# Optimization experiments

Hardware: AMD Instinct MI355X
Metric: run time of the kernel (lower is better)

The kernel has to match this reference:

```python
import jax, jax.numpy as jnp
import numpy as np

E = 1024
H = 8
D = E // H
WINDOW = 256
EPS = 1e-5


def layernorm(x, w, b):
    mu = jnp.mean(x, axis=-1, keepdims=True)
    var = jnp.mean((x - mu) ** 2, axis=-1, keepdims=True)
    return (x - mu) * jax.lax.rsqrt(var + EPS) * w + b


def setup_inputs() -> dict:
    key = jax.random.key(0)
    ks = jax.random.split(key, 12)
    B, T = 2, 2048
    s = 1.0 / np.sqrt(E)
    return {
        "x": jax.random.normal(ks[0], (B, T, E), jnp.float32),
        "ln1_w": jnp.ones((E,), jnp.float32),
        "ln1_b": jnp.zeros((E,), jnp.float32),
        "ln2_w": jnp.ones((E,), jnp.float32),
        "ln2_b": jnp.zeros((E,), jnp.float32),
        "in_proj_w": jax.random.normal(ks[1], (3 * E, E), jnp.float32) * s,
        "in_proj_b": jnp.zeros((3 * E,), jnp.float32),
        "out_w": jax.random.normal(ks[2], (E, E), jnp.float32) * s,
        "out_b": jnp.zeros((E,), jnp.float32),
        "w1": jax.random.normal(ks[3], (4 * E, E), jnp.float32) * s,
        "b1": jnp.zeros((4 * E,), jnp.float32),
        "w2": jax.random.normal(ks[4], (E, 4 * E), jnp.float32) * (1.0 / np.sqrt(4 * E)),
        "b2": jnp.zeros((E,), jnp.float32),
    }


def reference(x, ln1_w, ln1_b, ln2_w, ln2_b, in_proj_w, in_proj_b, out_w, out_b, w1, b1, w2, b2):
    B, T, _ = x.shape
    h = layernorm(x, ln1_w, ln1_b)
    # qkv projection: torch Linear is x @ W.T + b
    qkv = h @ in_proj_w.T + in_proj_b  # [B,T,3E]
    q, k, v = jnp.split(qkv, 3, axis=-1)
    q = q.reshape(B, T, H, D).transpose(0, 2, 1, 3)  # [B,H,T,D]
    k = k.reshape(B, T, H, D).transpose(0, 2, 1, 3)
    v = v.reshape(B, T, H, D).transpose(0, 2, 1, 3)
    scores = jnp.einsum("bhqd,bhkd->bhqk", q, k) / np.sqrt(D)
    idx = jnp.arange(T)
    row = idx[:, None]
    col = idx[None, :]
    # masked where future (col>row) OR outside window (col < row - WINDOW)
    allowed = (col <= row) & (col >= row - WINDOW)
    scores = jnp.where(allowed, scores, -jnp.inf)
    attn = jax.nn.softmax(scores, axis=-1)
    out = jnp.einsum("bhqk,bhkd->bhqd", attn, v)  # [B,H,T,D]
    out = out.transpose(0, 2, 1, 3).reshape(B, T, E)
    out = out @ out_w.T + out_b
    h2 = x + out
    m = layernorm(h2, ln2_w, ln2_b)
    m = jax.nn.relu(m @ w1.T + b1) @ w2.T + b2
    return h2 + m
```

## Files before the change

### kernel.cpp

```cpp
#include <hip/hip_runtime.h>

#define TOK 4096
#define EMB 1024

typedef __attribute__((ext_vector_type(8))) short s16x8;
typedef __attribute__((ext_vector_type(4))) float f32x4;

__device__ __forceinline__ unsigned short f2bf(float f) {
  union { float f; unsigned int u; } v; v.f = f;
  unsigned int r = v.u + 0x7FFFu + ((v.u >> 16) & 1u);
  return (unsigned short)(r >> 16);
}
__device__ __forceinline__ float bf2f(unsigned short u) {
  union { unsigned int u; float f; } v; v.u = ((unsigned int)u) << 16; return v.f;
}

#define GLOAD_LDS16(g, l) __builtin_amdgcn_global_load_lds( \
    (const __attribute__((address_space(1))) void*)(g), \
    (__attribute__((address_space(3))) void*)(l), 16, 0, 0)

template<int RELU, int PART, int NT>
__global__ __launch_bounds__(512)
void gemm256(const unsigned short* __restrict__ A,
             const unsigned short* __restrict__ B,
             const float* __restrict__ bias,
             unsigned short* __restrict__ C, int M, int N, int K)
{
  __shared__ unsigned short lds[2][2][128 * 128];
  const int tid = threadIdx.x;
  const int lane = tid & 63;
  const int w = tid >> 6;
  const int wr = w >> 2, wc = w & 3;
  const int l15 = lane & 15, lhi = lane >> 4;
  const int nbm = M >> 8;
  const int bm = blockIdx.x % nbm, bn = blockIdx.x / nbm;
  const int m0 = bm << 8, n0 = bn << 8;
  const int k0 = blockIdx.y * (NT * 64);

  const char* Abase = (const char*)(A + (size_t)m0 * K) + (size_t)k0 * 2;
  const char* Bbase = (const char*)(B + (size_t)n0 * K) + (size_t)k0 * 2;
  const size_t rowb = (size_t)K * 2;

  const int srt = tid >> 3;
  const int sccx = ((tid & 7) << 4) ^ ((srt & 7) << 4);
  const char* gA = Abase + (size_t)srt * rowb + sccx;
  const char* gB = Bbase + (size_t)srt * rowb + sccx;

  auto STAGE_A = [&](int ktl, int h, int p) {
    char* d = (char*)&lds[0][0][0] + p * 32768 + h * 16384 + (w << 10);
    const char* g = gA + (size_t)(h * 128) * rowb + ktl * 128;
    GLOAD_LDS16(g, d);
    GLOAD_LDS16(g + 64 * rowb, d + 8192);
  };
  auto STAGE_B = [&](int ktl, int h, int p) {
    char* d = (char*)&lds[1][0][0] + p * 32768 + h * 16384 + (w << 10);
    const char* g = gB + (size_t)(h * 128) * rowb + ktl * 128;
    GLOAD_LDS16(g, d);
    GLOAD_LDS16(g + 64 * rowb, d + 8192);
  };

  const int rdxor = (l15 & 7) << 4;
  const char* pA0 = (const char*)&lds[0][0][0] + (wr * 128 + l15) * 128 + ((0 * 64 + lhi * 16) ^ rdxor);
  const char* pA1 = (const char*)&lds[0][0][0] + (wr * 128 + l15) * 128 + ((1 * 64 + lhi * 16) ^ rdxor);
  const char* pB0 = (const char*)&lds[1][0][0] + (wc * 64 + l15) * 128 + ((0 * 64 + lhi * 16) ^ rdxor);
  const char* pB1 = (const char*)&lds[1][0][0] + (wc * 64 + l15) * 128 + ((1 * 64 + lhi * 16) ^ rdxor);

  f32x4 acc[8][4];
#pragma unroll
  for (int mf = 0; mf < 8; ++mf)
#pragma unroll
    for (int nf = 0; nf < 4; ++nf)
#pragma unroll
      for (int j = 0; j < 4; ++j) acc[mf][nf][j] = 0.f;

  STAGE_A(0, 0, 0); STAGE_A(0, 1, 0);
  STAGE_B(0, 0, 0); STAGE_B(0, 1, 0);
  STAGE_A(1, 0, 1); STAGE_A(1, 1, 1);
  STAGE_B(1, 0, 1);
  asm volatile("s_waitcnt vmcnt(6)" ::: "memory");
  __builtin_amdgcn_s_barrier();

  s16x8 af[8][2], bf[4][2];

#pragma unroll
  for (int kt = 0; kt < NT; ++kt) {
    const int P = (kt & 1) << 15;
    const int p = kt & 1;

#pragma unroll
    for (int mi = 0; mi < 4; ++mi) {
      af[mi][0] = *(const s16x8*)(pA0 + mi * 2048 + P);
      af[mi][1] = *(const s16x8*)(pA1 + mi * 2048 + P);
    }
#pragma unroll
    for (int ni = 0; ni < 2; ++ni) {
      bf[ni][0] = *(const s16x8*)(pB0 + ni * 2048 + P);
      bf[ni][1] = *(const s16x8*)(pB1 + ni * 2048 + P);
    }
#pragma unroll
    for (int mi = 4; mi < 8; ++mi) {
      af[mi][0] = *(const s16x8*)(pA0 + mi * 2048 + P);
      af[mi][1] = *(const s16x8*)(pA1 + mi * 2048 + P);
    }
#pragma unroll
    for (int ni = 2; ni < 4; ++ni) {
      bf[ni][0] = *(const s16x8*)(pB0 + ni * 2048 + P);
      bf[ni][1] = *(const s16x8*)(pB1 + ni * 2048 + P);
    }

    if (kt + 1 < NT) STAGE_B(kt + 1, 1, p ^ 1);

    __builtin_amdgcn_s_setprio(1);
#pragma unroll
    for (int mi = 0; mi < 4; ++mi)
#pragma unroll
      for (int ni = 0; ni < 2; ++ni)
#pragma unroll
        for (int ks = 0; ks < 2; ++ks)
          acc[mi][ni] = __builtin_amdgcn_mfma_f32_16x16x32_bf16(af[mi][ks], bf[ni][ks], acc[mi][ni], 0, 0, 0);
#pragma unroll
    for (int mi = 4; mi < 8; ++mi)
#pragma unroll
      for (int ni = 0; ni < 2; ++ni)
#pragma unroll
        for (int ks = 0; ks < 2; ++ks)
          acc[mi][ni] = __builtin_amdgcn_mfma_f32_16x16x32_bf16(af[mi][ks], bf[ni][ks], acc[mi][ni], 0, 0, 0);
#pragma unroll
    for (int mi = 0; mi < 4; ++mi)
#pragma unroll
      for (int ni = 2; ni < 4; ++ni)
#pragma unroll
        for (int ks = 0; ks < 2; ++ks)
          acc[mi][ni] = __builtin_amdgcn_mfma_f32_16x16x32_bf16(af[mi][ks], bf[ni][ks], acc[mi][ni], 0, 0, 0);
#pragma unroll
    for (int mi = 4; mi < 8; ++mi)
#pragma unroll
      for (int ni = 2; ni < 4; ++ni)
#pragma unroll
        for (int ks = 0; ks < 2; ++ks)
          acc[mi][ni] = __builtin_amdgcn_mfma_f32_16x16x32_bf16(af[mi][ks], bf[ni][ks], acc[mi][ni], 0, 0, 0);
    __builtin_amdgcn_s_setprio(0);

    __builtin_amdgcn_s_barrier();

    if (kt + 2 < NT) {
      STAGE_A(kt + 2, 0, p);
      STAGE_A(kt + 2, 1, p);
      STAGE_B(kt + 2, 0, p);
    }

    if (kt + 1 < NT) {
      if (kt + 2 < NT) asm volatile("s_waitcnt vmcnt(6)" ::: "memory");
      else             asm volatile("s_waitcnt vmcnt(0)" ::: "memory");
      __builtin_amdgcn_s_barrier();
    }
  }

  unsigned short* Cw = PART ? C + (size_t)blockIdx.y * M * N : C;
#pragma unroll
  for (int mf = 0; mf < 8; ++mf) {
    const int row = m0 + wr * 128 + mf * 16 + lhi * 4;
#pragma unroll
    for (int nf = 0; nf < 4; ++nf) {
      const int col = n0 + wc * 64 + nf * 16 + l15;
      const float bv = PART ? 0.f : bias[col];
#pragma unroll
      for (int j = 0; j < 4; ++j) {
        float v = acc[mf][nf][j] + bv;
        if (RELU) v = fmaxf(v, 0.f);
        Cw[(size_t)(row + j) * N + col] = f2bf(v);
      }
    }
  }
}

__global__ __launch_bounds__(256)
void reduce_add(const unsigned short* __restrict__ part, const float* __restrict__ res,
                const float* __restrict__ bias, float* __restrict__ out,
                int MN, int N, int S)
{
  const int i4 = (blockIdx.x * 256 + threadIdx.x) * 4;
  if (i4 >= MN) return;
  const int col = i4 & (N - 1);
  float4 v = *(const float4*)(res + i4);
  v.x += bias[col]; v.y += bias[col + 1]; v.z += bias[col + 2]; v.w += bias[col + 3];
  for (int s = 0; s < S; ++s) {
    const ushort4 p = *(const ushort4*)(part + (size_t)s * MN + i4);
    v.x += bf2f(p.x); v.y += bf2f(p.y); v.z += bf2f(p.z); v.w += bf2f(p.w);
  }
  *(float4*)(out + i4) = v;
}

__global__ __launch_bounds__(256)
void reduce_ln(const unsigned short* __restrict__ part, const float* __restrict__ x,
               const float* __restrict__ ob, const float* __restrict__ ln_w,
               const float* __restrict__ ln_b, float* __restrict__ h2,
               unsigned short* __restrict__ m_in, int S)
{
  const int row = blockIdx.x;
  const int t = threadIdx.x;
  const size_t off = (size_t)row * EMB + t * 4;
  float4 v = *(const float4*)(x + off);
  const float4 obv = ((const float4*)ob)[t];
  v.x += obv.x; v.y += obv.y; v.z += obv.z; v.w += obv.w;
  for (int s = 0; s < S; ++s) {
    const ushort4 p = *(const ushort4*)(part + (size_t)s * TOK * EMB + off);
    v.x += bf2f(p.x); v.y += bf2f(p.y); v.z += bf2f(p.z); v.w += bf2f(p.w);
  }
  *(float4*)(h2 + off) = v;

  float s1 = v.x + v.y + v.z + v.w;
  float s2 = v.x * v.x + v.y * v.y + v.z * v.z + v.w * v.w;
#pragma unroll
  for (int o = 1; o < 64; o <<= 1) { s1 += __shfl_xor(s1, o); s2 += __shfl_xor(s2, o); }
  __shared__ float red[8];
  if ((t & 63) == 0) { red[t >> 6] = s1; red[4 + (t >> 6)] = s2; }
  __syncthreads();
  s1 = red[0] + red[1] + red[2] + red[3];
  s2 = red[4] + red[5] + red[6] + red[7];
  const float mu = s1 * (1.f / EMB);
  const float rs = rsqrtf(s2 * (1.f / EMB) - mu * mu + 1e-5f);
  const float4 wv = ((const float4*)ln_w)[t];
  const float4 bv = ((const float4*)ln_b)[t];
  ushort4 o;
  o.x = f2bf((v.x - mu) * rs * wv.x + bv.x);
  o.y = f2bf((v.y - mu) * rs * wv.y + bv.y);
  o.z = f2bf((v.z - mu) * rs * wv.z + bv.z);
  o.w = f2bf((v.w - mu) * rs * wv.w + bv.w);
  ((ushort4*)(m_in + (size_t)row * EMB))[t] = o;
}

__global__ __launch_bounds__(256)
void ln_bf16(const float* __restrict__ x, const float* __restrict__ wt,
             const float* __restrict__ bs, unsigned short* __restrict__ out)
{
  const int row = blockIdx.x;
  const int t = threadIdx.x;
  const float4 v = ((const float4*)(x + (size_t)row * EMB))[t];
  float s = v.x + v.y + v.z + v.w;
  float s2 = v.x * v.x + v.y * v.y + v.z * v.z + v.w * v.w;
#pragma unroll
  for (int off = 1; off < 64; off <<= 1) { s += __shfl_xor(s, off); s2 += __shfl_xor(s2, off); }
  __shared__ float red[8];
  if ((t & 63) == 0) { red[t >> 6] = s; red[4 + (t >> 6)] = s2; }
  __syncthreads();
  s = red[0] + red[1] + red[2] + red[3];
  s2 = red[4] + red[5] + red[6] + red[7];
  const float mu = s * (1.f / EMB);
  const float rs = rsqrtf(s2 * (1.f / EMB) - mu * mu + 1e-5f);
  const float4 wv = ((const float4*)wt)[t];
  const float4 bv = ((const float4*)bs)[t];
  ushort4 o;
  o.x = f2bf((v.x - mu) * rs * wv.x + bv.x);
  o.y = f2bf((v.y - mu) * rs * wv.y + bv.y);
  o.z = f2bf((v.z - mu) * rs * wv.z + bv.z);
  o.w = f2bf((v.w - mu) * rs * wv.w + bv.w);
  ((ushort4*)(out + (size_t)row * EMB))[t] = o;
}

#define Q0 786432
#define Q1 (Q0 + 262144)
#define Q2 (Q1 + 1048576)
#define Q3 (Q2 + 1048576)
__global__ __launch_bounds__(256)
void cvt4(const float* __restrict__ s0, const float* __restrict__ s1,
          const float* __restrict__ s2, const float* __restrict__ s3,
          unsigned short* __restrict__ d0, unsigned short* __restrict__ d1,
          unsigned short* __restrict__ d2, unsigned short* __restrict__ d3)
{
  const int i = blockIdx.x * 256 + threadIdx.x;
  const float* s; unsigned short* d; int off;
  if (i < Q0)      { s = s0; d = d0; off = i; }
  else if (i < Q1) { s = s1; d = d1; off = i - Q0; }
  else if (i < Q2) { s = s2; d = d2; off = i - Q1; }
  else             { s = s3; d = d3; off = i - Q2; }
  const float4 v = ((const float4*)s)[off];
  ushort4 o;
  o.x = f2bf(v.x); o.y = f2bf(v.y); o.z = f2bf(v.z); o.w = f2bf(v.w);
  ((ushort4*)d)[off] = o;
}

__global__ __launch_bounds__(256)
void attn_win(const unsigned short* __restrict__ qkv, unsigned short* __restrict__ aout)
{
  __shared__ unsigned short Ks[64 * 136];
  __shared__ unsigned short Vt[128 * 72];
  __shared__ unsigned short Ps[4 * 16 * 72];
  const int bh = blockIdx.y;
  const int b = bh >> 3, hh = bh & 7;
  const int q0 = blockIdx.x << 6;
  const int tid = threadIdx.x, lane = tid & 63, w = tid >> 6;
  const int l15 = lane & 15, lhi = lane >> 4;
  const size_t base = (size_t)b * 2048 * 3072;

  s16x8 qf[4];
  {
    const unsigned short* qp = qkv + base + (size_t)(q0 + w * 16 + l15) * 3072 + hh * 128 + lhi * 8;
#pragma unroll
    for (int ks = 0; ks < 4; ++ks) qf[ks] = *(const s16x8*)(qp + ks * 32);
  }

  f32x4 o[8];
#pragma unroll
  for (int n = 0; n < 8; ++n)
#pragma unroll
    for (int j = 0; j < 4; ++j) o[n][j] = 0.f;
  float mrow[4] = {-1e30f, -1e30f, -1e30f, -1e30f};
  float lrow[4] = {0.f, 0.f, 0.f, 0.f};

  for (int t = 0; t < 5; ++t) {
    const int kt0 = q0 - 256 + t * 64;
    if (kt0 < 0) continue;
    __syncthreads();
    {
      const unsigned short* kg = qkv + base + (size_t)kt0 * 3072 + 1024 + hh * 128;
#pragma unroll
      for (int i = 0; i < 4; ++i) {
        const int c = tid + i * 256;
        const int r = c >> 4, cc = (c & 15) << 3;
        *(s16x8*)(Ks + r * 136 + cc) = *(const s16x8*)(kg + (size_t)r * 3072 + cc);
      }
      const unsigned short* vg = qkv + base + (size_t)kt0 * 3072 + 2048 + hh * 128;
#pragma unroll
      for (int i = 0; i < 2; ++i) {
        const int c = tid + i * 256;
        const int r2 = c >> 4, cc = (c & 15) << 3;
        s16x8 v0 = *(const s16x8*)(vg + (size_t)(2 * r2) * 3072 + cc);
        s16x8 v1 = *(const s16x8*)(vg + (size_t)(2 * r2 + 1) * 3072 + cc);
#pragma unroll
        for (int jj = 0; jj < 8; ++jj) {
          unsigned int pk = (unsigned int)(unsigned short)v0[jj] |
                            ((unsigned int)(unsigned short)v1[jj] << 16);
          *(unsigned int*)(Vt + (cc + jj) * 72 + 2 * r2) = pk;
        }
      }
    }
    __syncthreads();

    f32x4 s[4];
#pragma unroll
    for (int n = 0; n < 4; ++n)
#pragma unroll
      for (int j = 0; j < 4; ++j) s[n][j] = 0.f;
#pragma unroll
    for (int ks = 0; ks < 4; ++ks) {
#pragma unroll
      for (int n = 0; n < 4; ++n) {
        s16x8 kf = *(const s16x8*)(Ks + (n * 16 + l15) * 136 + ks * 32 + lhi * 8);
        s[n] = __builtin_amdgcn_mfma_f32_16x16x32_bf16(qf[ks], kf, s[n], 0, 0, 0);
      }
    }
    const bool mlo = (t == 0);
    const bool mhi = (kt0 == q0);
#pragma unroll
    for (int n = 0; n < 4; ++n) {
      const int kcol = n * 16 + l15;
#pragma unroll
      for (int j = 0; j < 4; ++j) {
        const int qrow = w * 16 + lhi * 4 + j;
        float v = s[n][j] * 0.08838834764831845f;
        if ((mlo && kcol < qrow) || (mhi && kcol > qrow)) v = -1e30f;
        s[n][j] = v;
      }
    }
    float alpha[4];
#pragma unroll
    for (int j = 0; j < 4; ++j) {
      float mx = fmaxf(fmaxf(s[0][j], s[1][j]), fmaxf(s[2][j], s[3][j]));
#pragma unroll
      for (int off = 1; off < 16; off <<= 1) mx = fmaxf(mx, __shfl_xor(mx, off));
      const float mn = fmaxf(mrow[j], mx);
      alpha[j] = __expf(mrow[j] - mn);
      mrow[j] = mn;
    }
    float rowsum[4] = {0.f, 0.f, 0.f, 0.f};
#pragma unroll
    for (int n = 0; n < 4; ++n)
#pragma unroll
      for (int j = 0; j < 4; ++j) {
        const float p = __expf(s[n][j] - mrow[j]);
        rowsum[j] += p;
        Ps[(w * 16 + lhi * 4 + j) * 72 + n * 16 + l15] = f2bf(p);
      }
#pragma unroll
    for (int j = 0; j < 4; ++j) {
      float rs = rowsum[j];
#pragma unroll
      for (int off = 1; off < 16; off <<= 1) rs += __shfl_xor(rs, off);
      lrow[j] = lrow[j] * alpha[j] + rs;
    }
#pragma unroll
    for (int n = 0; n < 8; ++n)
#pragma unroll
      for (int j = 0; j < 4; ++j) o[n][j] *= alpha[j];
#pragma unroll
    for (int ks = 0; ks < 2; ++ks) {
      const s16x8 pf = *(const s16x8*)(Ps + (w * 16 + l15) * 72 + ks * 32 + lhi * 8);
#pragma unroll
      for (int n = 0; n < 8; ++n) {
        const s16x8 vf = *(const s16x8*)(Vt + (n * 16 + l15) * 72 + ks * 32 + lhi * 8);
        o[n] = __builtin_amdgcn_mfma_f32_16x16x32_bf16(pf, vf, o[n], 0, 0, 0);
      }
    }
  }
  unsigned short* op = aout + (size_t)(b * 2048 + q0 + w * 16) * 1024 + hh * 128;
#pragma unroll
  for (int n = 0; n < 8; ++n)
#pragma unroll
    for (int j = 0; j < 4; ++j)
      op[(size_t)(lhi * 4 + j) * 1024 + n * 16 + l15] = f2bf(o[n][j] / lrow[j]);
}

extern "C" void kernel_launch(void* const* d_in, const int* in_sizes, int n_in,
                              void* d_out, int out_size, void* d_ws, size_t ws_size,
                              hipStream_t stream)
{
  (void)in_sizes; (void)n_in; (void)out_size; (void)ws_size;
  const float* x         = (const float*)d_in[0];
  const float* ln1_w     = (const float*)d_in[1];
  const float* ln1_b     = (const float*)d_in[2];
  const float* ln2_w     = (const float*)d_in[3];
  const float* ln2_b     = (const float*)d_in[4];
  const float* in_proj_w = (const float*)d_in[5];
  const float* in_proj_b = (const float*)d_in[6];
  const float* out_w     = (const float*)d_in[7];
  const float* out_b     = (const float*)d_in[8];
  const float* w1        = (const float*)d_in[9];
  const float* b1        = (const float*)d_in[10];
  const float* w2        = (const float*)d_in[11];
  const float* b2        = (const float*)d_in[12];
  float* out = (float*)d_out;

  char* ws = (char*)d_ws;
  unsigned short* h    = (unsigned short*)(ws);
  unsigned short* wqkv = (unsigned short*)(ws + (8u << 20));
  unsigned short* wout = (unsigned short*)(ws + (14u << 20));
  unsigned short* w1b  = (unsigned short*)(ws + (16u << 20));
  unsigned short* w2b  = (unsigned short*)(ws + (24u << 20));
  unsigned short* qkv  = (unsigned short*)(ws + (32u << 20));
  unsigned short* aout = (unsigned short*)(ws + (56u << 20));
  float*          h2   = (float*)(ws + (64u << 20));
  unsigned short* m_in = (unsigned short*)(ws + (80u << 20));
  unsigned short* act  = (unsigned short*)(ws + (88u << 20));
  unsigned short* part_op = (unsigned short*)(ws + (88u << 20));
  unsigned short* part_m2 = (unsigned short*)(ws + (32u << 20));

  cvt4<<<dim3(Q3 / 256), 256, 0, stream>>>(in_proj_w, out_w, w1, w2, wqkv, wout, w1b, w2b);
  ln_bf16<<<dim3(TOK), 256, 0, stream>>>(x, ln1_w, ln1_b, h);

  gemm256<0, 0, 16><<<dim3(16 * 12), 512, 0, stream>>>(h, wqkv, in_proj_b, qkv, 4096, 3072, 1024);
  attn_win<<<dim3(32, 16), 256, 0, stream>>>(qkv, aout);

  gemm256<0, 1, 4><<<dim3(16 * 4, 4), 512, 0, stream>>>(aout, wout, nullptr, part_op, 4096, 1024, 1024);
  reduce_ln<<<dim3(TOK), 256, 0, stream>>>(part_op, x, out_b, ln2_w, ln2_b, h2, m_in, 4);

  gemm256<1, 0, 16><<<dim3(16 * 16), 512, 0, stream>>>(m_in, w1b, b1, act, 4096, 4096, 1024);

  gemm256<0, 1, 16><<<dim3(16 * 4, 4), 512, 0, stream>>>(act, w2b, nullptr, part_m2, 4096, 1024, 4096);
  reduce_add<<<dim3(4096 * 1024 / 4 / 256), 256, 0, stream>>>(part_m2, h2, b2, out, 4096 * 1024, 1024, 4);
}
```

Before: 191.4 us.

## Replace split-K partial buffers and reduce kernels with fp32 atomic accumulation

The split-K GEMMs for the output projection and the second MLP layer now atomically add fp32 partials straight into pre-initialised destinations (h2 and out), replacing bf16 partial buffers and separate reduction passes. The residual plus bias initialisation moves into the LayerNorm kernels, so the final reduce_add kernel is removed and reduce_ln becomes a plain LayerNorm over h2. This drops a launch and the round trip through the partial buffers, in exchange for many scattered global atomics and a summation order that is no longer deterministic.

```diff
diff --git a/kernel.cpp b/kernel.cpp
--- a/kernel.cpp
+++ b/kernel.cpp
@@ -19,12 +19,12 @@
     (const __attribute__((address_space(1))) void*)(g), \
     (__attribute__((address_space(3))) void*)(l), 16, 0, 0)
 
-template<int RELU, int PART, int NT>
+template<int RELU, int MODE, int NT>
 __global__ __launch_bounds__(512)
 void gemm256(const unsigned short* __restrict__ A,
              const unsigned short* __restrict__ B,
              const float* __restrict__ bias,
-             unsigned short* __restrict__ C, int M, int N, int K)
+             void* __restrict__ C, int M, int N, int K)
 {
   __shared__ unsigned short lds[2][2][128 * 128];
   const int tid = threadIdx.x;
@@ -156,58 +156,75 @@
     }
   }
 
-  unsigned short* Cw = PART ? C + (size_t)blockIdx.y * M * N : C;
 #pragma unroll
   for (int mf = 0; mf < 8; ++mf) {
     const int row = m0 + wr * 128 + mf * 16 + lhi * 4;
 #pragma unroll
     for (int nf = 0; nf < 4; ++nf) {
       const int col = n0 + wc * 64 + nf * 16 + l15;
-      const float bv = PART ? 0.f : bias[col];
-#pragma unroll
-      for (int j = 0; j < 4; ++j) {
-        float v = acc[mf][nf][j] + bv;
-        if (RELU) v = fmaxf(v, 0.f);
-        Cw[(size_t)(row + j) * N + col] = f2bf(v);
+      if (MODE == 0) {
+        const float bv = bias[col];
+#pragma unroll
+        for (int j = 0; j < 4; ++j) {
+          float v = acc[mf][nf][j] + bv;
+          if (RELU) v = fmaxf(v, 0.f);
+          ((unsigned short*)C)[(size_t)(row + j) * N + col] = f2bf(v);
+        }
+      } else {
+#pragma unroll
+        for (int j = 0; j < 4; ++j)
+          atomicAdd((float*)C + (size_t)(row + j) * N + col, acc[mf][nf][j]);
       }
     }
   }
 }
 
 __global__ __launch_bounds__(256)
-void reduce_add(const unsigned short* __restrict__ part, const float* __restrict__ res,
-                const float* __restrict__ bias, float* __restrict__ out,
-                int MN, int N, int S)
-{
-  const int i4 = (blockIdx.x * 256 + threadIdx.x) * 4;
-  if (i4 >= MN) return;
-  const int col = i4 & (N - 1);
-  float4 v = *(const float4*)(res + i4);
-  v.x += bias[col]; v.y += bias[col + 1]; v.z += bias[col + 2]; v.w += bias[col + 3];
-  for (int s = 0; s < S; ++s) {
-    const ushort4 p = *(const ushort4*)(part + (size_t)s * MN + i4);
-    v.x += bf2f(p.x); v.y += bf2f(p.y); v.z += bf2f(p.z); v.w += bf2f(p.w);
-  }
-  *(float4*)(out + i4) = v;
-}
-
-__global__ __launch_bounds__(256)
-void reduce_ln(const unsigned short* __restrict__ part, const float* __restrict__ x,
-               const float* __restrict__ ob, const float* __restrict__ ln_w,
-               const float* __restrict__ ln_b, float* __restrict__ h2,
-               unsigned short* __restrict__ m_in, int S)
+void ln1_init(const float* __restrict__ x, const float* __restrict__ wt,
+              const float* __restrict__ bs, const float* __restrict__ ob,
+              unsigned short* __restrict__ out, float* __restrict__ h2i)
 {
   const int row = blockIdx.x;
   const int t = threadIdx.x;
-  const size_t off = (size_t)row * EMB + t * 4;
-  float4 v = *(const float4*)(x + off);
+  const float4 v = ((const float4*)(x + (size_t)row * EMB))[t];
   const float4 obv = ((const float4*)ob)[t];
-  v.x += obv.x; v.y += obv.y; v.z += obv.z; v.w += obv.w;
-  for (int s = 0; s < S; ++s) {
-    const ushort4 p = *(const ushort4*)(part + (size_t)s * TOK * EMB + off);
-    v.x += bf2f(p.x); v.y += bf2f(p.y); v.z += bf2f(p.z); v.w += bf2f(p.w);
-  }
-  *(float4*)(h2 + off) = v;
+  float4 hi;
+  hi.x = v.x + obv.x; hi.y = v.y + obv.y; hi.z = v.z + obv.z; hi.w = v.w + obv.w;
+  ((float4*)(h2i + (size_t)row * EMB))[t] = hi;
+
+  float s = v.x + v.y + v.z + v.w;
+  float s2 = v.x * v.x + v.y * v.y + v.z * v.z + v.w * v.w;
+#pragma unroll
+  for (int off = 1; off < 64; off <<= 1) { s += __shfl_xor(s, off); s2 += __shfl_xor(s2, off); }
+  __shared__ float red[8];
+  if ((t & 63) == 0) { red[t >> 6] = s; red[4 + (t >> 6)] = s2; }
+  __syncthreads();
+  s = red[0] + red[1] + red[2] + red[3];
+  s2 = red[4] + red[5] + red[6] + red[7];
+  const float mu = s * (1.f / EMB);
+  const float rs = rsqrtf(s2 * (1.f / EMB) - mu * mu + 1e-5f);
+  const float4 wv = ((const float4*)wt)[t];
+  const float4 bv = ((const float4*)bs)[t];
+  ushort4 o;
+  o.x = f2bf((v.x - mu) * rs * wv.x + bv.x);
+  o.y = f2bf((v.y - mu) * rs * wv.y + bv.y);
+  o.z = f2bf((v.z - mu) * rs * wv.z + bv.z);
+  o.w = f2bf((v.w - mu) * rs * wv.w + bv.w);
+  ((ushort4*)(out + (size_t)row * EMB))[t] = o;
+}
+
+__global__ __launch_bounds__(256)
+void ln2_init(const float* __restrict__ h2, const float* __restrict__ ln_w,
+              const float* __restrict__ ln_b, const float* __restrict__ b2,
+              unsigned short* __restrict__ m_in, float* __restrict__ out)
+{
+  const int row = blockIdx.x;
+  const int t = threadIdx.x;
+  const float4 v = ((const float4*)(h2 + (size_t)row * EMB))[t];
+  const float4 b2v = ((const float4*)b2)[t];
+  float4 oi;
+  oi.x = v.x + b2v.x; oi.y = v.y + b2v.y; oi.z = v.z + b2v.z; oi.w = v.w + b2v.w;
+  ((float4*)(out + (size_t)row * EMB))[t] = oi;
 
   float s1 = v.x + v.y + v.z + v.w;
   float s2 = v.x * v.x + v.y * v.y + v.z * v.z + v.w * v.w;
@@ -230,34 +247,6 @@
   ((ushort4*)(m_in + (size_t)row * EMB))[t] = o;
 }
 
-__global__ __launch_bounds__(256)
-void ln_bf16(const float* __restrict__ x, const float* __restrict__ wt,
-             const float* __restrict__ bs, unsigned short* __restrict__ out)
-{
-  const int row = blockIdx.x;
-  const int t = threadIdx.x;
-  const float4 v = ((const float4*)(x + (size_t)row * EMB))[t];
-  float s = v.x + v.y + v.z + v.w;
-  float s2 = v.x * v.x + v.y * v.y + v.z * v.z + v.w * v.w;
-#pragma unroll
-  for (int off = 1; off < 64; off <<= 1) { s += __shfl_xor(s, off); s2 += __shfl_xor(s2, off); }
-  __shared__ float red[8];
-  if ((t & 63) == 0) { red[t >> 6] = s; red[4 + (t >> 6)] = s2; }
-  __syncthreads();
-  s = red[0] + red[1] + red[2] + red[3];
-  s2 = red[4] + red[5] + red[6] + red[7];
-  const float mu = s * (1.f / EMB);
-  const float rs = rsqrtf(s2 * (1.f / EMB) - mu * mu + 1e-5f);
-  const float4 wv = ((const float4*)wt)[t];
-  const float4 bv = ((const float4*)bs)[t];
-  ushort4 o;
-  o.x = f2bf((v.x - mu) * rs * wv.x + bv.x);
-  o.y = f2bf((v.y - mu) * rs * wv.y + bv.y);
-  o.z = f2bf((v.z - mu) * rs * wv.z + bv.z);
-  o.w = f2bf((v.w - mu) * rs * wv.w + bv.w);
-  ((ushort4*)(out + (size_t)row * EMB))[t] = o;
-}
-
 #define Q0 786432
 #define Q1 (Q0 + 262144)
 #define Q2 (Q1 + 1048576)
@@ -442,20 +431,17 @@
   float*          h2   = (float*)(ws + (64u << 20));
   unsigned short* m_in = (unsigned short*)(ws + (80u << 20));
   unsigned short* act  = (unsigned short*)(ws + (88u << 20));
-  unsigned short* part_op = (unsigned short*)(ws + (88u << 20));
-  unsigned short* part_m2 = (unsigned short*)(ws + (32u << 20));
 
   cvt4<<<dim3(Q3 / 256), 256, 0, stream>>>(in_proj_w, out_w, w1, w2, wqkv, wout, w1b, w2b);
-  ln_bf16<<<dim3(TOK), 256, 0, stream>>>(x, ln1_w, ln1_b, h);
+  ln1_init<<<dim3(TOK), 256, 0, stream>>>(x, ln1_w, ln1_b, out_b, h, h2);
 
   gemm256<0, 0, 16><<<dim3(16 * 12), 512, 0, stream>>>(h, wqkv, in_proj_b, qkv, 4096, 3072, 1024);
   attn_win<<<dim3(32, 16), 256, 0, stream>>>(qkv, aout);
 
-  gemm256<0, 1, 4><<<dim3(16 * 4, 4), 512, 0, stream>>>(aout, wout, nullptr, part_op, 4096, 1024, 1024);
-  reduce_ln<<<dim3(TOK), 256, 0, stream>>>(part_op, x, out_b, ln2_w, ln2_b, h2, m_in, 4);
+  gemm256<0, 2, 4><<<dim3(16 * 4, 4), 512, 0, stream>>>(aout, wout, nullptr, h2, 4096, 1024, 1024);
+  ln2_init<<<dim3(TOK), 256, 0, stream>>>(h2, ln2_w, ln2_b, b2, m_in, out);
 
   gemm256<1, 0, 16><<<dim3(16 * 16), 512, 0, stream>>>(m_in, w1b, b1, act, 4096, 4096, 1024);
 
-  gemm256<0, 1, 16><<<dim3(16 * 4, 4), 512, 0, stream>>>(act, w2b, nullptr, part_m2, 4096, 1024, 4096);
-  reduce_add<<<dim3(4096 * 1024 / 4 / 256), 256, 0, stream>>>(part_m2, h2, b2, out, 4096 * 1024, 1024, 4);
-}
+  gemm256<0, 2, 16><<<dim3(16 * 4, 4), 512, 0, stream>>>(act, w2b, nullptr, out, 4096, 1024, 4096);
+}
```

Result: slower. 261.4 us (+36.6%).
